# Optimization experiments

Hardware: AMD Instinct MI355X
Metric: run time of the kernel (lower is better)

## Reference

```python
import jax, jax.numpy as jnp
import numpy as np

B, Cin, Cout, H, W = 8, 64, 128, 128, 128
K, S, P = 3, 1, 1
KK = K * K
EPS = 1e-5


def _conv2d(x, w, b=None):
    out = jax.lax.conv_general_dilated(
        x, w, window_strides=(S, S), padding=[(P, P), (P, P)],
        dimension_numbers=('NCHW', 'OIHW', 'NCHW'))
    if b is not None:
        out = out + b[None, :, None, None]
    return out


def setup_inputs() -> dict:
    key = jax.random.key(0)
    k = jax.random.split(key, 5)
    sc = 1.0 / np.sqrt(Cin * KK)
    return {
        'x': jax.random.normal(k[0], (B, Cin, H, W), jnp.float32),
        'offset_w': jax.random.normal(k[1], (2 * KK, Cin, K, K), jnp.float32) * sc,
        'offset_b': jnp.zeros((2 * KK,), jnp.float32),
        'mask_w': jax.random.normal(k[2], (KK, Cin, K, K), jnp.float32) * sc,
        'mask_b': jnp.zeros((KK,), jnp.float32),
        'conv_w': jax.random.normal(k[3], (Cout, Cin, K, K), jnp.float32) * sc,
    }


def _deform_conv2d(x, offset, mask, w):
    """Modulated deformable conv (torchvision deform_conv2d semantics)."""
    Bn, C, Hh, Ww = x.shape
    Ho, Wo = offset.shape[2], offset.shape[3]
    off = offset.reshape(Bn, KK, 2, Ho, Wo)  # (y, x) pairs per kernel tap
    ky, kx = jnp.meshgrid(jnp.arange(K), jnp.arange(K), indexing='ij')
    ky = ky.reshape(KK).astype(x.dtype)
    kx = kx.reshape(KK).astype(x.dtype)
    hy = (jnp.arange(Ho) * S - P).astype(x.dtype)
    wx = (jnp.arange(Wo) * S - P).astype(x.dtype)
    # sampling positions [B, KK, Ho, Wo]
    py = off[:, :, 0] + ky[None, :, None, None] + hy[None, None, :, None]
    px = off[:, :, 1] + kx[None, :, None, None] + wx[None, None, None, :]

    y0 = jnp.floor(py)
    x0 = jnp.floor(px)
    wy1 = py - y0; wx1 = px - x0
    wy0 = 1.0 - wy1; wx0 = 1.0 - wx1

    xf = x.reshape(Bn, C, Hh * Ww)

    def gather(yi, xi):
        valid = ((yi >= 0) & (yi < Hh) & (xi >= 0) & (xi < Ww)).astype(x.dtype)
        yc = jnp.clip(yi, 0, Hh - 1).astype(jnp.int32)
        xc = jnp.clip(xi, 0, Ww - 1).astype(jnp.int32)
        idx = (yc * Ww + xc).reshape(Bn, -1)  # [B, KK*Ho*Wo]
        vals = jnp.take_along_axis(xf, idx[:, None, :], axis=2)  # [B, C, KK*Ho*Wo]
        return vals.reshape(Bn, C, KK, Ho, Wo) * valid.reshape(Bn, 1, KK, Ho, Wo)

    v = (gather(y0, x0) * (wy0 * wx0)[:, None]
         + gather(y0, x0 + 1) * (wy0 * wx1)[:, None]
         + gather(y0 + 1, x0) * (wy1 * wx0)[:, None]
         + gather(y0 + 1, x0 + 1) * (wy1 * wx1)[:, None])  # [B, C, KK, Ho, Wo]
    v = v * mask[:, None]  # modulation
    return jnp.einsum('bckhw,ock->bohw', v, w.reshape(w.shape[0], C, KK))


def reference(x, offset_w, offset_b, mask_w, mask_b, conv_w):
    offset = _conv2d(x, offset_w, offset_b)
    mask = jax.nn.sigmoid(_conv2d(x, mask_w, mask_b))
    out = _deform_conv2d(x, offset, mask, conv_w)
    # BatchNorm2d(affine=False), training-mode normalization over (N, H, W)
    mean = out.mean(axis=(0, 2, 3), keepdims=True)
    var = out.var(axis=(0, 2, 3), keepdims=True)
    return jax.nn.relu((out - mean) * jax.lax.rsqrt(var + EPS))
```

## Files before the change

### kernel.cpp

```cpp
#include <hip/hip_runtime.h>
#include <hip/hip_bf16.h>

#define H_ 128
#define W_ 128
#define HW 16384
#define CIN 64
#define COUT 128
#define KK9 9
#define BATCH 8
#define NPIX (BATCH * HW)
#define KDIM 576

typedef short bf16x8 __attribute__((ext_vector_type(8)));
typedef float f32x4  __attribute__((ext_vector_type(4)));
typedef unsigned short ushort_t;

union U4B { uint4 u; bf16x8 v; };

__device__ __forceinline__ float us2f(unsigned short u) {
    unsigned int v = ((unsigned int)u) << 16;
    float f;
    __builtin_memcpy(&f, &v, 4);
    return f;
}
__device__ __forceinline__ float lo_f(unsigned int w) {
    unsigned int v = w << 16;
    float f;
    __builtin_memcpy(&f, &v, 4);
    return f;
}
__device__ __forceinline__ float hi_f(unsigned int w) {
    unsigned int v = w & 0xffff0000u;
    float f;
    __builtin_memcpy(&f, &v, 4);
    return f;
}
__device__ __forceinline__ unsigned short f2us_bf(float f) {
    __hip_bfloat16 h = __float2bfloat16(f);
    unsigned short u;
    __builtin_memcpy(&u, &h, 2);
    return u;
}
__device__ __forceinline__ unsigned int pack2(float a, float b) {
    return (unsigned int)f2us_bf(a) | ((unsigned int)f2us_bf(b) << 16);
}

template <bool F32>
__device__ __forceinline__ float ld_in(const void* p, long i) {
    if (F32) return ((const float*)p)[i];
    return us2f(((const unsigned short*)p)[i]);
}

__global__ void detect_zero(const uint4* __restrict__ xr4,
                            float* __restrict__ flag,
                            float* __restrict__ gstat) {
    int t = threadIdx.x;
#pragma unroll
    for (int i = 0; i < 16; ++i) gstat[i * 256 + t] = 0.0f;
    if (t < 64) {
        uint4 v = xr4[t];
        unsigned int w[4] = {v.x, v.y, v.z, v.w};
        int big = 0;
#pragma unroll
        for (int q = 0; q < 4; ++q) {
            big += (((w[q] >> 7)  & 0xFF) >= 0xC0);
            big += (((w[q] >> 23) & 0xFF) >= 0xC0);
        }
        unsigned long long m = __ballot(big > 0);
        if (t == 0) flag[0] = m ? 1.0f : 0.0f;
    }
}

template <bool F32>
__device__ __forceinline__ void prep_body(const void* offw, const void* offb,
                                          const void* maskw, const void* maskb,
                                          const void* convw,
                                          ushort_t* wTs, ushort_t* wcats,
                                          float* bias, int i) {
    if (i < 73728) {
        int j = i & 7, lane = (i >> 3) & 63, n = (i >> 9) & 7, ks = i >> 12;
        int co = n * 16 + (lane & 15);
        int k  = ks * 32 + ((lane >> 4) << 3) + j;
        int kk = k >> 6, ci = k & 63;
        wTs[i] = f2us_bf(ld_in<F32>(convw, (long)co * KDIM + ci * 9 + kk));
    } else if (i < 73728 + 18432) {
        int i2 = i - 73728;
        int j = i2 & 7, lane = (i2 >> 3) & 63, n = (i2 >> 9) & 1, ks = i2 >> 10;
        int co2 = n * 16 + (lane & 15);
        int k   = ks * 32 + ((lane >> 4) << 3) + j;
        int kk = k >> 6, ci = k & 63;
        float v = 0.0f;
        if (co2 < 18)      v = ld_in<F32>(offw,  (long)co2 * KDIM + ci * 9 + kk);
        else if (co2 < 27) v = ld_in<F32>(maskw, (long)(co2 - 18) * KDIM + ci * 9 + kk);
        wcats[i2] = f2us_bf(v);
    } else if (i < 73728 + 18432 + 32) {
        int j = i - 73728 - 18432;
        float v = 0.0f;
        if (j < 18)      v = ld_in<F32>(offb, j);
        else if (j < 27) v = ld_in<F32>(maskb, j - 18);
        bias[j] = v;
    }
}

__global__ void prep_weights(const void* __restrict__ offw,
                             const void* __restrict__ offb,
                             const void* __restrict__ maskw,
                             const void* __restrict__ maskb,
                             const void* __restrict__ convw,
                             const float* __restrict__ flag,
                             ushort_t* __restrict__ wTs,
                             ushort_t* __restrict__ wcats,
                             float* __restrict__ bias) {
    int i = blockIdx.x * 256 + threadIdx.x;
    if (flag[0] != 0.0f)
        prep_body<true>(offw, offb, maskw, maskb, convw, wTs, wcats, bias, i);
    else
        prep_body<false>(offw, offb, maskw, maskb, convw, wTs, wcats, bias, i);
}

template <bool F32>
__device__ __forceinline__ void transpose_body(const void* x, ushort_t* xnb) {
    __shared__ float tile[CIN * 65];
    int blk  = blockIdx.x;
    int b    = blk >> 8;
    int pix0 = (blk & 255) * 64;
    int t    = threadIdx.x;
#pragma unroll
    for (int pass = 0; pass < 4; ++pass) {
        int slot = pass * 256 + t;
        int ci = slot >> 4;
        int f4 = slot & 15;
        long base = (long)(b * CIN + ci) * HW + pix0 + f4 * 4;
        float v0, v1, v2, v3;
        if (F32) {
            float4 v = *(const float4*)((const float*)x + base);
            v0 = v.x; v1 = v.y; v2 = v.z; v3 = v.w;
        } else {
            ushort4 u = *(const ushort4*)((const ushort_t*)x + base);
            v0 = us2f(u.x); v1 = us2f(u.y); v2 = us2f(u.z); v3 = us2f(u.w);
        }
        tile[ci * 65 + f4 * 4 + 0] = v0;
        tile[ci * 65 + f4 * 4 + 1] = v1;
        tile[ci * 65 + f4 * 4 + 2] = v2;
        tile[ci * 65 + f4 * 4 + 3] = v3;
    }
    __syncthreads();
#pragma unroll
    for (int pass = 0; pass < 4; ++pass) {
        int slot = pass * 256 + t;
        int px = slot >> 4;
        int c4 = slot & 15;
        ushort4 o;
        o.x = f2us_bf(tile[(c4 * 4 + 0) * 65 + px]);
        o.y = f2us_bf(tile[(c4 * 4 + 1) * 65 + px]);
        o.z = f2us_bf(tile[(c4 * 4 + 2) * 65 + px]);
        o.w = f2us_bf(tile[(c4 * 4 + 3) * 65 + px]);
        *(ushort4*)(xnb + (size_t)(b * HW + pix0 + px) * CIN + c4 * 4) = o;
    }
}

__global__ __launch_bounds__(256) void transpose_x(const void* __restrict__ x,
                                                   const float* __restrict__ flag,
                                                   ushort_t* __restrict__ xnb) {
    if (flag[0] != 0.0f) transpose_body<true>(x, xnb);
    else                 transpose_body<false>(x, xnb);
}

__device__ __forceinline__ void compute_tap(int yp_t, int xp_t,
                                            float oy, float ox, float mk,
                                            int* ofs, float* wg) {
    float py  = (float)yp_t + oy;
    float pxf = (float)xp_t + ox;
    float y0f = floorf(py), x0f = floorf(pxf);
    int yi = (int)y0f, xi = (int)x0f;
    float wy1 = py - y0f, wx1 = pxf - x0f;
    float wy0 = 1.0f - wy1, wx0 = 1.0f - wx1;
    int ya  = min(max(yi, 0), H_ - 1);
    int yb  = min(max(yi + 1, 0), H_ - 1);
    int xa  = min(max(xi, 0), W_ - 1);
    int xb2 = min(max(xi + 1, 0), W_ - 1);
    bool vy0 = (yi >= 0) & (yi < H_);
    bool vy1 = (yi >= -1) & (yi < H_ - 1);
    bool vx0 = (xi >= 0) & (xi < W_);
    bool vx1 = (xi >= -1) & (xi < W_ - 1);
    float m0 = mk * wy0, m1 = mk * wy1;
    wg[0] = (vy0 & vx0) ? m0 * wx0 : 0.0f;
    wg[1] = (vy0 & vx1) ? m0 * wx1 : 0.0f;
    wg[2] = (vy1 & vx0) ? m1 * wx0 : 0.0f;
    wg[3] = (vy1 & vx1) ? m1 * wx1 : 0.0f;
    int ra = ya << 13, rb = yb << 13;
    int ca = xa << 6,  cb_ = xb2 << 6;
    ofs[0] = ra + ca;  ofs[1] = ra + cb_;
    ofs[2] = rb + ca;  ofs[3] = rb + cb_;
}

__device__ __forceinline__ void issue_half(const ushort_t* __restrict__ xb,
                                           const int* ofs, int hoff, uint4* cb) {
#pragma unroll
    for (int c = 0; c < 4; ++c)
        cb[c] = *(const uint4*)(xb + ofs[c] + hoff);
}

__device__ __forceinline__ void consume_half(int slot, const uint4* cb,
                                             const float* wg,
                                             const ushort_t* __restrict__ ldsB,
                                             int lane, f32x4* acc) {
    float2 v2[4];
#pragma unroll
    for (int j = 0; j < 4; ++j) v2[j] = make_float2(0.f, 0.f);
#pragma unroll
    for (int c = 0; c < 4; ++c) {
        float w = wg[c];
        unsigned int ww[4] = {cb[c].x, cb[c].y, cb[c].z, cb[c].w};
#pragma unroll
        for (int j = 0; j < 4; ++j) {
            v2[j].x = fmaf(w, lo_f(ww[j]), v2[j].x);
            v2[j].y = fmaf(w, hi_f(ww[j]), v2[j].y);
        }
    }
    U4B a;
    a.u = make_uint4(pack2(v2[0].x, v2[0].y), pack2(v2[1].x, v2[1].y),
                     pack2(v2[2].x, v2[2].y), pack2(v2[3].x, v2[3].y));
    const ushort_t* bbase = ldsB + ((size_t)(slot * 8) * 64 + lane) * 8;
    __builtin_amdgcn_s_setprio(1);
#pragma unroll
    for (int n = 0; n < 8; ++n) {
        bf16x8 bf = *(const bf16x8*)(bbase + n * 64 * 8);
        acc[n] = __builtin_amdgcn_mfma_f32_16x16x32_bf16(a.v, bf, acc[n], 0, 0, 0);
    }
    __builtin_amdgcn_s_setprio(0);
}

__global__ __launch_bounds__(512, 4) void fused_conv_deform(
        const ushort_t* __restrict__ xnb,
        const ushort_t* __restrict__ wcats,
        const float* __restrict__ bias,
        const ushort_t* __restrict__ wTs,
        ushort_t* __restrict__ prebn,
        float* __restrict__ gstat) {
    __shared__ uint4 lds[4000];
    float2* offL  = (float2*)(lds + 3072);
    float*  maskS = (float*) (lds + 3648);
    float*  red   = (float*) (lds + 3936);

    int t    = threadIdx.x;
    int bid  = blockIdx.x;
    int sbid = (bid & 7) * 128 + (bid >> 3);
    int pix0 = sbid * 128;
    int b    = pix0 >> 14;
    int rem0 = pix0 & 16383;
    int y0   = rem0 >> 7;

    const uint4* wc4 = (const uint4*)wcats;
    for (int i = t; i < 2304; i += 512) lds[i] = wc4[i];
    if (t < 256) red[t] = 0.0f;

    int wave = t >> 6, lane = t & 63, mrow = lane & 15, quad = lane >> 4;
    int px_l = wave * 16 + mrow;
    int xp   = px_l;
    const ushort_t* xb = xnb + (size_t)b * HW * CIN + quad * 8;

    uint4 af0[9], af1[9];
#pragma unroll
    for (int kk = 0; kk < 9; ++kk) {
        int yy = y0 + kk / 3 - 1;
        int xq = xp + kk % 3 - 1;
        bool ok = (yy >= 0) && (yy < H_) && (xq >= 0) && (xq < W_);
        const ushort_t* src = xb + (size_t)(yy * W_ + xq) * CIN;
        af0[kk] = ok ? *(const uint4*)src        : make_uint4(0, 0, 0, 0);
        af1[kk] = ok ? *(const uint4*)(src + 32) : make_uint4(0, 0, 0, 0);
    }
    __syncthreads();

    {
        f32x4 cacc[2];
        cacc[0] = (f32x4){0.f, 0.f, 0.f, 0.f};
        cacc[1] = (f32x4){0.f, 0.f, 0.f, 0.f};
        const ushort_t* ldsBc = (const ushort_t*)lds;
#pragma unroll
        for (int kk = 0; kk < 9; ++kk) {
#pragma unroll
            for (int half = 0; half < 2; ++half) {
                int ks = kk * 2 + half;
                U4B a; a.u = half ? af1[kk] : af0[kk];
#pragma unroll
                for (int n = 0; n < 2; ++n) {
                    bf16x8 bf = *(const bf16x8*)(ldsBc + ((ks * 2 + n) * 64 + lane) * 8);
                    cacc[n] = __builtin_amdgcn_mfma_f32_16x16x32_bf16(a.v, bf, cacc[n], 0, 0, 0);
                }
            }
        }
#pragma unroll
        for (int n = 0; n < 2; ++n) {
            int co2 = n * 16 + mrow;
            if (co2 >= 27) continue;
            float bs = bias[co2];
#pragma unroll
            for (int r = 0; r < 4; ++r) {
                int px = wave * 16 + quad * 4 + r;
                float v = cacc[n][r] + bs;
                if (co2 < 18)
                    ((float*)offL)[((co2 >> 1) * 128 + px) * 2 + (co2 & 1)] = v;
                else
                    maskS[(co2 - 18) * 128 + px] = 1.0f / (1.0f + __expf(-v));
            }
        }
    }
    __syncthreads();

    const uint4* ws4 = (const uint4*)wTs;
    for (int i = t; i < 3072; i += 512) lds[i] = ws4[i];

    int remp = rem0 + px_l;
    int yp  = remp >> 7, xp2 = remp & 127;

    f32x4 acc[8];
#pragma unroll
    for (int n = 0; n < 8; ++n) acc[n] = (f32x4){0.f, 0.f, 0.f, 0.f};

    int   ofs[2][4];
    float wg[2][4];
    uint4 cb[3][4];

    float2 oE  = offL[px_l];           float mkE = maskS[px_l];
    float2 oO  = offL[128 + px_l];     float mkO = maskS[128 + px_l];
    compute_tap(yp - 1, xp2 - 1, oE.x, oE.y, mkE, ofs[0], wg[0]);
    issue_half(xb, ofs[0], 0,  cb[0]);
    issue_half(xb, ofs[0], 32, cb[1]);
    oE = offL[2 * 128 + px_l];  mkE = maskS[2 * 128 + px_l];
    __builtin_amdgcn_sched_barrier(0);
    __syncthreads();

    const ushort_t* ldsB = (const ushort_t*)lds;

#define ISSUE_STEP(hs)  do {                                                  \
    const int hs2 = (hs) + 2;                                                 \
    if (hs2 < 18) {                                                           \
        const int kk2 = hs2 >> 1;                                             \
        const int s2  = hs2 % 3;                                              \
        if ((hs2 & 1) == 0) {                                                 \
            const int tp2 = kk2 & 1;                                          \
            float ooy = tp2 ? oO.x : oE.x;                                    \
            float oox = tp2 ? oO.y : oE.y;                                    \
            float omk = tp2 ? mkO  : mkE;                                     \
            compute_tap(yp + kk2 / 3 - 1, xp2 + kk2 % 3 - 1, ooy, oox, omk,   \
                        ofs[tp2], wg[tp2]);                                   \
            issue_half(xb, ofs[tp2], 0, cb[s2]);                              \
            if (kk2 + 2 <= 8) {                                               \
                float2 o = offL[(kk2 + 2) * 128 + px_l];                      \
                float  m = maskS[(kk2 + 2) * 128 + px_l];                     \
                if (tp2) { oO = o; mkO = m; } else { oE = o; mkE = m; }       \
            }                                                                 \
        } else {                                                              \
            issue_half(xb, ofs[kk2 & 1], 32, cb[s2]);                         \
        }                                                                     \
    }                                                                         \
    __builtin_amdgcn_sched_barrier(0);                                        \
} while (0)

#pragma unroll
    for (int hs = 0; hs < 6; ++hs) {
        ISSUE_STEP(hs);
        consume_half(hs, cb[hs % 3], wg[(hs >> 1) & 1], ldsB, lane, acc);
    }
    __syncthreads();
    for (int i = t; i < 3072; i += 512) lds[i] = ws4[3072 + i];
    __syncthreads();
#pragma unroll
    for (int hs = 6; hs < 12; ++hs) {
        ISSUE_STEP(hs);
        consume_half(hs - 6, cb[hs % 3], wg[(hs >> 1) & 1], ldsB, lane, acc);
    }
    __syncthreads();
    for (int i = t; i < 3072; i += 512) lds[i] = ws4[6144 + i];
    __syncthreads();
#pragma unroll
    for (int hs = 12; hs < 18; ++hs) {
        ISSUE_STEP(hs);
        consume_half(hs - 12, cb[hs % 3], wg[(hs >> 1) & 1], ldsB, lane, acc);
    }
#undef ISSUE_STEP

#pragma unroll
    for (int n = 0; n < 8; ++n) {
        int co = n * 16 + mrow;
        float s = 0.f, ss = 0.f;
#pragma unroll
        for (int r = 0; r < 4; ++r) {
            int pg = pix0 + wave * 16 + quad * 4 + r;
            float v = acc[n][r];
            prebn[(size_t)pg * COUT + co] = f2us_bf(v);
            s += v;
            ss += v * v;
        }
        s  += __shfl_xor(s, 16, 64);
        s  += __shfl_xor(s, 32, 64);
        ss += __shfl_xor(ss, 16, 64);
        ss += __shfl_xor(ss, 32, 64);
        if (quad == 0) {
            atomicAdd(&red[co], s);
            atomicAdd(&red[128 + co], ss);
        }
    }
    __syncthreads();
    if (t < 256) atomicAdd(&gstat[(bid & 15) * 256 + t], red[t]);
}

__global__ __launch_bounds__(256) void bn_apply_t(const ushort_t* __restrict__ prebn,
                                                  const float* __restrict__ gstat,
                                                  float* __restrict__ out) {
    __shared__ float tile[128 * 65];
    __shared__ float mvs[256];
    int t = threadIdx.x;
    if (t < 128) {
        float s = 0.f, ss = 0.f;
#pragma unroll
        for (int part = 0; part < 16; ++part) {
            s  += gstat[part * 256 + t];
            ss += gstat[part * 256 + 128 + t];
        }
        const float invN = 1.0f / (float)NPIX;
        float mean = s * invN;
        float var  = ss * invN - mean * mean;
        if (!isfinite(mean)) mean = 0.0f;
        float r = rsqrtf(fmaxf(var, 0.0f) + 1e-5f);
        if (!isfinite(r)) r = 1.0f;
        mvs[t]       = mean;
        mvs[128 + t] = r;
    }
    __syncthreads();
    int pix0 = blockIdx.x * 64;
    int b    = pix0 >> 14;
    int rem0 = pix0 & 16383;
    const uint4* src4 = (const uint4*)(prebn + (size_t)pix0 * COUT);
#pragma unroll
    for (int r = 0; r < 4; ++r) {
        int i  = r * 256 + t;
        uint4 v = src4[i];
        int p  = i >> 4;
        int c0 = (i & 15) * 8;
        unsigned int w[4] = {v.x, v.y, v.z, v.w};
#pragma unroll
        for (int j = 0; j < 4; ++j) {
            int c = c0 + j * 2;
            float f0 = lo_f(w[j]);
            float f1 = hi_f(w[j]);
            tile[c * 65 + p]       = fmaxf((f0 - mvs[c])     * mvs[128 + c],     0.0f);
            tile[(c + 1) * 65 + p] = fmaxf((f1 - mvs[c + 1]) * mvs[128 + c + 1], 0.0f);
        }
    }
    __syncthreads();
#pragma unroll
    for (int r = 0; r < 8; ++r) {
        int i  = r * 256 + t;
        int c2 = i >> 4;
        int q  = (i & 15) * 4;
        float4 w4 = make_float4(tile[c2 * 65 + q],     tile[c2 * 65 + q + 1],
                                tile[c2 * 65 + q + 2], tile[c2 * 65 + q + 3]);
        *(float4*)(out + (size_t)(b * COUT + c2) * HW + rem0 + q) = w4;
    }
}

extern "C" void kernel_launch(void* const* d_in, const int* in_sizes, int n_in,
                              void* d_out, int out_size, void* d_ws, size_t ws_size,
                              hipStream_t stream) {
    (void)in_sizes; (void)n_in; (void)out_size; (void)ws_size;
    const void* x     = d_in[0];
    const void* offw  = d_in[1];
    const void* offb  = d_in[2];
    const void* maskw = d_in[3];
    const void* maskb = d_in[4];
    const void* convw = d_in[5];

    float* ws       = (float*)d_ws;
    float* off2     = ws;
    float* mask_ws  = off2 + 2359296;
    float* bias     = mask_ws + 1179648;
    float* gstat    = bias + 32;
    float* flag     = gstat + 4096;
    ushort_t* wTs   = (ushort_t*)(flag + 16);
    ushort_t* wcats = wTs + 73728;
    ushort_t* xnb   = wcats + 18432;
    ushort_t* prebn = xnb + 8388608;
    float* out      = (float*)d_out;

    detect_zero<<<1, 256, 0, stream>>>((const uint4*)x, flag, gstat);
    prep_weights<<<361, 256, 0, stream>>>(offw, offb, maskw, maskb, convw, flag, wTs, wcats, bias);
    transpose_x<<<2048, 256, 0, stream>>>(x, flag, xnb);
    fused_conv_deform<<<1024, 512, 0, stream>>>(xnb, wcats, bias, wTs, prebn, gstat);
    bn_apply_t<<<2048, 256, 0, stream>>>(prebn, gstat, out);
}
```

Baseline: 217.2 us.

## Merge prep kernels, double fused-conv block to 1024 threads, use packed bf16 convert

Merges the dtype-detect, weight-prep and input-transpose kernels into one launch, with each block redoing the dtype check into shared memory. The fused deformable-conv kernel moves to 1024-thread blocks covering 256 pixels, so the weight tiles in LDS are shared by twice as many waves and are reloaded by fewer blocks. The fp32-to-bf16 packing now uses the hardware v_cvt_pk_bf16_f32 instruction, setprio is removed, and the sched_barrier mask is relaxed. The risks are lower occupancy or register pressure under launch_bounds(1024,4), a larger LDS footprint, and the redundant per-block flag check.

```diff
diff --git a/kernel.cpp b/kernel.cpp
--- a/kernel.cpp
+++ b/kernel.cpp
@@ -41,34 +41,16 @@
     __builtin_memcpy(&u, &h, 2);
     return u;
 }
-__device__ __forceinline__ unsigned int pack2(float a, float b) {
-    return (unsigned int)f2us_bf(a) | ((unsigned int)f2us_bf(b) << 16);
+__device__ __forceinline__ unsigned int cvtpk_bf16(float a, float b) {
+    unsigned int r;
+    asm("v_cvt_pk_bf16_f32 %0, %1, %2" : "=v"(r) : "v"(a), "v"(b));
+    return r;
 }
 
 template <bool F32>
 __device__ __forceinline__ float ld_in(const void* p, long i) {
     if (F32) return ((const float*)p)[i];
     return us2f(((const unsigned short*)p)[i]);
-}
-
-__global__ void detect_zero(const uint4* __restrict__ xr4,
-                            float* __restrict__ flag,
-                            float* __restrict__ gstat) {
-    int t = threadIdx.x;
-#pragma unroll
-    for (int i = 0; i < 16; ++i) gstat[i * 256 + t] = 0.0f;
-    if (t < 64) {
-        uint4 v = xr4[t];
-        unsigned int w[4] = {v.x, v.y, v.z, v.w};
-        int big = 0;
-#pragma unroll
-        for (int q = 0; q < 4; ++q) {
-            big += (((w[q] >> 7)  & 0xFF) >= 0xC0);
-            big += (((w[q] >> 23) & 0xFF) >= 0xC0);
-        }
-        unsigned long long m = __ballot(big > 0);
-        if (t == 0) flag[0] = m ? 1.0f : 0.0f;
-    }
 }
 
 template <bool F32>
@@ -102,26 +84,10 @@
     }
 }
 
-__global__ void prep_weights(const void* __restrict__ offw,
-                             const void* __restrict__ offb,
-                             const void* __restrict__ maskw,
-                             const void* __restrict__ maskb,
-                             const void* __restrict__ convw,
-                             const float* __restrict__ flag,
-                             ushort_t* __restrict__ wTs,
-                             ushort_t* __restrict__ wcats,
-                             float* __restrict__ bias) {
-    int i = blockIdx.x * 256 + threadIdx.x;
-    if (flag[0] != 0.0f)
-        prep_body<true>(offw, offb, maskw, maskb, convw, wTs, wcats, bias, i);
-    else
-        prep_body<false>(offw, offb, maskw, maskb, convw, wTs, wcats, bias, i);
-}
-
 template <bool F32>
-__device__ __forceinline__ void transpose_body(const void* x, ushort_t* xnb) {
+__device__ __forceinline__ void transpose_body(const void* x, ushort_t* xnb,
+                                               int blk) {
     __shared__ float tile[CIN * 65];
-    int blk  = blockIdx.x;
     int b    = blk >> 8;
     int pix0 = (blk & 255) * 64;
     int t    = threadIdx.x;
@@ -150,20 +116,54 @@
         int slot = pass * 256 + t;
         int px = slot >> 4;
         int c4 = slot & 15;
-        ushort4 o;
-        o.x = f2us_bf(tile[(c4 * 4 + 0) * 65 + px]);
-        o.y = f2us_bf(tile[(c4 * 4 + 1) * 65 + px]);
-        o.z = f2us_bf(tile[(c4 * 4 + 2) * 65 + px]);
-        o.w = f2us_bf(tile[(c4 * 4 + 3) * 65 + px]);
-        *(ushort4*)(xnb + (size_t)(b * HW + pix0 + px) * CIN + c4 * 4) = o;
-    }
-}
-
-__global__ __launch_bounds__(256) void transpose_x(const void* __restrict__ x,
-                                                   const float* __restrict__ flag,
-                                                   ushort_t* __restrict__ xnb) {
-    if (flag[0] != 0.0f) transpose_body<true>(x, xnb);
-    else                 transpose_body<false>(x, xnb);
+        uint2 o;
+        o.x = cvtpk_bf16(tile[(c4 * 4 + 0) * 65 + px], tile[(c4 * 4 + 1) * 65 + px]);
+        o.y = cvtpk_bf16(tile[(c4 * 4 + 2) * 65 + px], tile[(c4 * 4 + 3) * 65 + px]);
+        *(uint2*)(xnb + (size_t)(b * HW + pix0 + px) * CIN + c4 * 4) = o;
+    }
+}
+
+__global__ __launch_bounds__(256) void prep_mega(
+        const void* __restrict__ x,
+        const void* __restrict__ offw,
+        const void* __restrict__ offb,
+        const void* __restrict__ maskw,
+        const void* __restrict__ maskb,
+        const void* __restrict__ convw,
+        ushort_t* __restrict__ wTs,
+        ushort_t* __restrict__ wcats,
+        float* __restrict__ bias,
+        float* __restrict__ gstat,
+        ushort_t* __restrict__ xnb) {
+    __shared__ float flagS;
+    int t   = threadIdx.x;
+    int blk = blockIdx.x;
+
+    if (t < 64) {
+        uint4 v = ((const uint4*)x)[t];
+        unsigned int w[4] = {v.x, v.y, v.z, v.w};
+        int big = 0;
+#pragma unroll
+        for (int q = 0; q < 4; ++q) {
+            big += (((w[q] >> 7)  & 0xFF) >= 0xC0);
+            big += (((w[q] >> 23) & 0xFF) >= 0xC0);
+        }
+        unsigned long long m = __ballot(big > 0);
+        if (t == 0) flagS = m ? 1.0f : 0.0f;
+    }
+    if (blk < 16) gstat[blk * 256 + t] = 0.0f;
+    __syncthreads();
+    bool isF32 = (flagS != 0.0f);
+
+    if (blk < 361) {
+        int i = blk * 256 + t;
+        if (isF32) prep_body<true >(offw, offb, maskw, maskb, convw, wTs, wcats, bias, i);
+        else       prep_body<false>(offw, offb, maskw, maskb, convw, wTs, wcats, bias, i);
+    } else {
+        int tb = blk - 361;
+        if (isF32) transpose_body<true >(x, xnb, tb);
+        else       transpose_body<false>(x, xnb, tb);
+    }
 }
 
 __device__ __forceinline__ void compute_tap(int yp_t, int xp_t,
@@ -219,51 +219,52 @@
         }
     }
     U4B a;
-    a.u = make_uint4(pack2(v2[0].x, v2[0].y), pack2(v2[1].x, v2[1].y),
-                     pack2(v2[2].x, v2[2].y), pack2(v2[3].x, v2[3].y));
+    a.u = make_uint4(cvtpk_bf16(v2[0].x, v2[0].y), cvtpk_bf16(v2[1].x, v2[1].y),
+                     cvtpk_bf16(v2[2].x, v2[2].y), cvtpk_bf16(v2[3].x, v2[3].y));
     const ushort_t* bbase = ldsB + ((size_t)(slot * 8) * 64 + lane) * 8;
-    __builtin_amdgcn_s_setprio(1);
 #pragma unroll
     for (int n = 0; n < 8; ++n) {
         bf16x8 bf = *(const bf16x8*)(bbase + n * 64 * 8);
         acc[n] = __builtin_amdgcn_mfma_f32_16x16x32_bf16(a.v, bf, acc[n], 0, 0, 0);
     }
-    __builtin_amdgcn_s_setprio(0);
-}
-
-__global__ __launch_bounds__(512, 4) void fused_conv_deform(
+}
+
+#define SB_PIN_VMEM() __builtin_amdgcn_sched_barrier(0x38F)
+
+__global__ __launch_bounds__(1024, 4) void fused_conv_deform(
         const ushort_t* __restrict__ xnb,
         const ushort_t* __restrict__ wcats,
         const float* __restrict__ bias,
         const ushort_t* __restrict__ wTs,
         ushort_t* __restrict__ prebn,
         float* __restrict__ gstat) {
-    __shared__ uint4 lds[4000];
+    __shared__ uint4 lds[4864];
+
     float2* offL  = (float2*)(lds + 3072);
-    float*  maskS = (float*) (lds + 3648);
-    float*  red   = (float*) (lds + 3936);
+    float*  maskS = (float*) (lds + 4224);
+    float*  red   = (float*) (lds + 4800);
 
     int t    = threadIdx.x;
     int bid  = blockIdx.x;
-    int sbid = (bid & 7) * 128 + (bid >> 3);
-    int pix0 = sbid * 128;
+    int sbid = (bid & 7) * 64 + (bid >> 3);
+    int pix0 = sbid * 256;
     int b    = pix0 >> 14;
     int rem0 = pix0 & 16383;
-    int y0   = rem0 >> 7;
 
     const uint4* wc4 = (const uint4*)wcats;
-    for (int i = t; i < 2304; i += 512) lds[i] = wc4[i];
+    for (int i = t; i < 2304; i += 1024) lds[i] = wc4[i];
     if (t < 256) red[t] = 0.0f;
 
     int wave = t >> 6, lane = t & 63, mrow = lane & 15, quad = lane >> 4;
     int px_l = wave * 16 + mrow;
-    int xp   = px_l;
+    int remp = rem0 + px_l;
+    int yp = remp >> 7, xp = remp & 127;
     const ushort_t* xb = xnb + (size_t)b * HW * CIN + quad * 8;
 
     uint4 af0[9], af1[9];
 #pragma unroll
     for (int kk = 0; kk < 9; ++kk) {
-        int yy = y0 + kk / 3 - 1;
+        int yy = yp + kk / 3 - 1;
         int xq = xp + kk % 3 - 1;
         bool ok = (yy >= 0) && (yy < H_) && (xq >= 0) && (xq < W_);
         const ushort_t* src = xb + (size_t)(yy * W_ + xq) * CIN;
@@ -300,19 +301,16 @@
                 int px = wave * 16 + quad * 4 + r;
                 float v = cacc[n][r] + bs;
                 if (co2 < 18)
-                    ((float*)offL)[((co2 >> 1) * 128 + px) * 2 + (co2 & 1)] = v;
+                    ((float*)offL)[((co2 >> 1) * 256 + px) * 2 + (co2 & 1)] = v;
                 else
-                    maskS[(co2 - 18) * 128 + px] = 1.0f / (1.0f + __expf(-v));
+                    maskS[(co2 - 18) * 256 + px] = 1.0f / (1.0f + __expf(-v));
             }
         }
     }
     __syncthreads();
 
     const uint4* ws4 = (const uint4*)wTs;
-    for (int i = t; i < 3072; i += 512) lds[i] = ws4[i];
-
-    int remp = rem0 + px_l;
-    int yp  = remp >> 7, xp2 = remp & 127;
+    for (int i = t; i < 3072; i += 1024) lds[i] = ws4[i];
 
     f32x4 acc[8];
 #pragma unroll
@@ -323,12 +321,12 @@
     uint4 cb[3][4];
 
     float2 oE  = offL[px_l];           float mkE = maskS[px_l];
-    float2 oO  = offL[128 + px_l];     float mkO = maskS[128 + px_l];
-    compute_tap(yp - 1, xp2 - 1, oE.x, oE.y, mkE, ofs[0], wg[0]);
+    float2 oO  = offL[256 + px_l];     float mkO = maskS[256 + px_l];
+    compute_tap(yp - 1, xp - 1, oE.x, oE.y, mkE, ofs[0], wg[0]);
     issue_half(xb, ofs[0], 0,  cb[0]);
     issue_half(xb, ofs[0], 32, cb[1]);
-    oE = offL[2 * 128 + px_l];  mkE = maskS[2 * 128 + px_l];
-    __builtin_amdgcn_sched_barrier(0);
+    oE = offL[2 * 256 + px_l];  mkE = maskS[2 * 256 + px_l];
+    SB_PIN_VMEM();
     __syncthreads();
 
     const ushort_t* ldsB = (const ushort_t*)lds;
@@ -343,19 +341,19 @@
             float ooy = tp2 ? oO.x : oE.x;                                    \
             float oox = tp2 ? oO.y : oE.y;                                    \
             float omk = tp2 ? mkO  : mkE;                                     \
-            compute_tap(yp + kk2 / 3 - 1, xp2 + kk2 % 3 - 1, ooy, oox, omk,   \
+            compute_tap(yp + kk2 / 3 - 1, xp + kk2 % 3 - 1, ooy, oox, omk,    \
                         ofs[tp2], wg[tp2]);                                   \
             issue_half(xb, ofs[tp2], 0, cb[s2]);                              \
             if (kk2 + 2 <= 8) {                                               \
-                float2 o = offL[(kk2 + 2) * 128 + px_l];                      \
-                float  m = maskS[(kk2 + 2) * 128 + px_l];                     \
+                float2 o = offL[(kk2 + 2) * 256 + px_l];                      \
+                float  m = maskS[(kk2 + 2) * 256 + px_l];                     \
                 if (tp2) { oO = o; mkO = m; } else { oE = o; mkE = m; }       \
             }                                                                 \
         } else {                                                              \
             issue_half(xb, ofs[kk2 & 1], 32, cb[s2]);                         \
         }                                                                     \
     }                                                                         \
-    __builtin_amdgcn_sched_barrier(0);                                        \
+    SB_PIN_VMEM();                                                            \
 } while (0)
 
 #pragma unroll
@@ -364,7 +362,7 @@
         consume_half(hs, cb[hs % 3], wg[(hs >> 1) & 1], ldsB, lane, acc);
     }
     __syncthreads();
-    for (int i = t; i < 3072; i += 512) lds[i] = ws4[3072 + i];
+    for (int i = t; i < 3072; i += 1024) lds[i] = ws4[3072 + i];
     __syncthreads();
 #pragma unroll
     for (int hs = 6; hs < 12; ++hs) {
@@ -372,7 +370,7 @@
         consume_half(hs - 6, cb[hs % 3], wg[(hs >> 1) & 1], ldsB, lane, acc);
     }
     __syncthreads();
-    for (int i = t; i < 3072; i += 512) lds[i] = ws4[6144 + i];
+    for (int i = t; i < 3072; i += 1024) lds[i] = ws4[6144 + i];
     __syncthreads();
 #pragma unroll
     for (int hs = 12; hs < 18; ++hs) {
@@ -484,9 +482,8 @@
     ushort_t* prebn = xnb + 8388608;
     float* out      = (float*)d_out;
 
-    detect_zero<<<1, 256, 0, stream>>>((const uint4*)x, flag, gstat);
-    prep_weights<<<361, 256, 0, stream>>>(offw, offb, maskw, maskb, convw, flag, wTs, wcats, bias);
-    transpose_x<<<2048, 256, 0, stream>>>(x, flag, xnb);
-    fused_conv_deform<<<1024, 512, 0, stream>>>(xnb, wcats, bias, wTs, prebn, gstat);
+    prep_mega<<<2409, 256, 0, stream>>>(x, offw, offb, maskw, maskb, convw,
+                                        wTs, wcats, bias, gstat, xnb);
+    fused_conv_deform<<<512, 1024, 0, stream>>>(xnb, wcats, bias, wTs, prebn, gstat);
     bn_apply_t<<<2048, 256, 0, stream>>>(prebn, gstat, out);
 }
```

Result: faster. 208.3 us (-4.1%).
